# Kernel optimization log

Hardware: AMD Instinct MI355X
Metric: run time of the kernel (lower is better)

Reference implementation:

```python
import jax, jax.numpy as jnp
import numpy as np

N = 131072
IN_DIM = 12
HID = 256
NUM_LAYERS = 10
OUT_DIM = 3


def _xavier(key, fan_in, fan_out, gain):
    bound = gain * jnp.sqrt(6.0 / (fan_in + fan_out))
    return jax.random.uniform(key, (fan_in, fan_out), jnp.float32, -bound, bound)


def setup_inputs() -> dict:
    key = jax.random.key(0)
    ks = jax.random.split(key, 12)
    x = jax.random.normal(ks[0], (N, IN_DIM), jnp.float32)
    W0 = _xavier(ks[1], IN_DIM, HID, 5.0)
    b0 = jnp.zeros((HID,), jnp.float32)
    Ws = jnp.stack([_xavier(ks[2 + i], HID, HID, 5.0) for i in range(NUM_LAYERS - 1)])
    bs = jnp.zeros((NUM_LAYERS - 1, HID), jnp.float32)
    Wout = _xavier(ks[11], HID, OUT_DIM, 1.0)
    bout = jnp.zeros((OUT_DIM,), jnp.float32)
    return {"x": x, "W0": W0, "b0": b0, "Ws": Ws, "bs": bs, "Wout": Wout, "bout": bout}


def _act(h, i):
    m = i % 4
    if m == 0:
        return jnp.sin(h)
    if m == 1:
        return jnp.cos(h)
    if m == 2:
        return jnp.exp(-h * h)  # gaussian
    return jnp.tanh(h)


def reference(x, W0, b0, Ws, bs, Wout, bout):
    h = _act(x @ W0 + b0, 0)
    for i in range(1, NUM_LAYERS):  # small fixed layer loop
        h = _act(h @ Ws[i - 1] + bs[i - 1], i)
    return jax.nn.sigmoid(h @ Wout + bout)  # (N, 3) in [0, 1]
```

## Files before the change

kernel.cpp:

```cpp
#include <hip/hip_runtime.h>
#include <type_traits>

#define HID 256
#define PTS 64
typedef unsigned short ushort_t;
typedef unsigned int uint_t;
typedef __attribute__((ext_vector_type(8))) _Float16 half8v;
typedef __attribute__((ext_vector_type(4))) float f32x4;

#define LO_SCALE   4096.0f
#define LO_INV     0.000244140625f

__device__ __forceinline__ ushort_t h_bits(_Float16 h) { return __builtin_bit_cast(ushort_t, h); }

template <int M>
__device__ __forceinline__ float act(float z) {
    if constexpr (M == 0) return __sinf(z);
    else if constexpr (M == 1) return __cosf(z);
    else if constexpr (M == 2) return __expf(-z * z);
    else { float e = __expf(2.0f * z); return 1.0f - 2.0f / (e + 1.0f); }
}

#define NFRAG (9 * 8 * 16)
#define PREP_THREADS (NFRAG * 64)

__global__ void prep_w(const float* __restrict__ Ws,
                       _Float16* __restrict__ WHI, _Float16* __restrict__ WLO) {
    int t = blockIdx.x * 256 + threadIdx.x;
    if (t >= PREP_THREADS) return;
    int l  = t & 63;
    int f  = t >> 6;
    int ct = f & 15;
    int kt = (f >> 4) & 7;
    int L  = f >> 7;
    int col = ct * 16 + (l & 15);
    int kb  = kt * 32 + (l >> 4) * 8;
    const float* Wp = Ws + (size_t)L * 65536;
    _Float16* oh = WHI + (size_t)t * 8;
    _Float16* ol = WLO + (size_t)t * 8;
    #pragma unroll
    for (int j = 0; j < 8; ++j) {
        float wv = Wp[(size_t)(kb + j) * 256 + col];
        _Float16 hi = (_Float16)wv;
        oh[j] = hi;
        ol[j] = (_Float16)((wv - (float)hi) * LO_SCALE);
    }
}

__global__ __launch_bounds__(512, 4) void cppn_mfma(
    const float* __restrict__ x,
    const float* __restrict__ W0,
    const float* __restrict__ b0,
    const float* __restrict__ bs,
    const float* __restrict__ Wout,
    const float* __restrict__ bout,
    const _Float16* __restrict__ WHI,
    const _Float16* __restrict__ WLO,
    float* __restrict__ out,
    int n)
{
    __shared__ ushort_t ha[64 * 256];
    __shared__ ushort_t hb[64 * 256];

    const int tid = threadIdx.x;
    const int l   = tid & 63;
    const int w   = tid >> 6;
    const long p0 = (long)blockIdx.x * PTS;

    {
        const int p  = l;
        const long pg = p0 + p;
        float xv[12];
        if (pg < n) {
            const float4* xr = (const float4*)(x + pg * 12);
            float4 a = xr[0], b = xr[1], c = xr[2];
            xv[0]=a.x; xv[1]=a.y; xv[2]=a.z;  xv[3]=a.w;
            xv[4]=b.x; xv[5]=b.y; xv[6]=b.z;  xv[7]=b.w;
            xv[8]=c.x; xv[9]=c.y; xv[10]=c.z; xv[11]=c.w;
        } else {
            #pragma unroll
            for (int k = 0; k < 12; ++k) xv[k] = 0.0f;
        }
        const int jb = w * 32;
        float z[32];
        #pragma unroll
        for (int jj = 0; jj < 32; ++jj) z[jj] = b0[jb + jj];
        #pragma unroll
        for (int k = 0; k < 12; ++k) {
            const float a = xv[k];
            #pragma unroll
            for (int jj = 0; jj < 32; ++jj)
                z[jj] = fmaf(a, W0[k * HID + jb + jj], z[jj]);
        }
        const int swz = (p & 7) << 3;
        #pragma unroll
        for (int jj = 0; jj < 32; jj += 2) {
            float v0 = act<0>(z[jj]), v1 = act<0>(z[jj + 1]);
            _Float16 h0 = (_Float16)v0, h1 = (_Float16)v1;
            _Float16 l0 = (_Float16)((v0 - (float)h0) * LO_SCALE);
            _Float16 l1 = (_Float16)((v1 - (float)h1) * LO_SCALE);
            int ei = p * 256 + ((jb + jj) ^ swz);
            *(uint_t*)&ha[ei] = (uint_t)h_bits(h0) | ((uint_t)h_bits(h1) << 16);
            *(uint_t*)&hb[ei] = (uint_t)h_bits(l0) | ((uint_t)h_bits(l1) << 16);
        }
    }
    __syncthreads();

    const int lg   = l >> 4;
    const int lm   = l & 15;
    const int aswz = (l & 7) << 3;
    const int ab[4] = { (0*16+lm)*256, (1*16+lm)*256, (2*16+lm)*256, (3*16+lm)*256 };

    for (int Li = 0; Li < 9; ++Li) {
        const _Float16* __restrict__ WHL = WHI + (size_t)(Li * 8 * 16) * 512 + (size_t)l * 8;
        const _Float16* __restrict__ WLL = WLO + (size_t)(Li * 8 * 16) * 512 + (size_t)l * 8;

        f32x4 acc[4][2], accL[4][2];
        #pragma unroll
        for (int rt = 0; rt < 4; ++rt)
            #pragma unroll
            for (int c = 0; c < 2; ++c) {
                acc[rt][c]  = (f32x4){0.f, 0.f, 0.f, 0.f};
                accL[rt][c] = (f32x4){0.f, 0.f, 0.f, 0.f};
            }

        half8v bch[2], bcl[2];
        bch[0] = *(const half8v*)(WHL + (size_t)(w * 2 + 0) * 512);
        bch[1] = *(const half8v*)(WHL + (size_t)(w * 2 + 1) * 512);
        bcl[0] = *(const half8v*)(WLL + (size_t)(w * 2 + 0) * 512);
        bcl[1] = *(const half8v*)(WLL + (size_t)(w * 2 + 1) * 512);

        #pragma unroll 1
        for (int kt = 0; kt < 8; ++kt) {
            const int ktn = (kt + 1) & 7;
            half8v bnh[2], bnl[2];
            bnh[0] = *(const half8v*)(WHL + (size_t)(ktn * 16 + w * 2 + 0) * 512);
            bnh[1] = *(const half8v*)(WHL + (size_t)(ktn * 16 + w * 2 + 1) * 512);
            bnl[0] = *(const half8v*)(WLL + (size_t)(ktn * 16 + w * 2 + 0) * 512);
            bnl[1] = *(const half8v*)(WLL + (size_t)(ktn * 16 + w * 2 + 1) * 512);

            const int ke = (kt * 32 + lg * 8) ^ aswz;

            {
                half8v a_hi[2], a_lo[2];
                a_hi[0] = *(const half8v*)&ha[ab[0] + ke];
                a_hi[1] = *(const half8v*)&ha[ab[1] + ke];
                a_lo[0] = *(const half8v*)&hb[ab[0] + ke];
                a_lo[1] = *(const half8v*)&hb[ab[1] + ke];
                #pragma unroll
                for (int c = 0; c < 2; ++c)
                    #pragma unroll
                    for (int r = 0; r < 2; ++r)
                        acc[r][c] = __builtin_amdgcn_mfma_f32_16x16x32_f16(a_hi[r], bch[c], acc[r][c], 0, 0, 0);
                #pragma unroll
                for (int c = 0; c < 2; ++c)
                    #pragma unroll
                    for (int r = 0; r < 2; ++r)
                        accL[r][c] = __builtin_amdgcn_mfma_f32_16x16x32_f16(a_hi[r], bcl[c], accL[r][c], 0, 0, 0);
                #pragma unroll
                for (int c = 0; c < 2; ++c)
                    #pragma unroll
                    for (int r = 0; r < 2; ++r)
                        accL[r][c] = __builtin_amdgcn_mfma_f32_16x16x32_f16(a_lo[r], bch[c], accL[r][c], 0, 0, 0);
            }
            {
                half8v a_hi[2], a_lo[2];
                a_hi[0] = *(const half8v*)&ha[ab[2] + ke];
                a_hi[1] = *(const half8v*)&ha[ab[3] + ke];
                a_lo[0] = *(const half8v*)&hb[ab[2] + ke];
                a_lo[1] = *(const half8v*)&hb[ab[3] + ke];
                #pragma unroll
                for (int c = 0; c < 2; ++c)
                    #pragma unroll
                    for (int r = 0; r < 2; ++r)
                        acc[2+r][c] = __builtin_amdgcn_mfma_f32_16x16x32_f16(a_hi[r], bch[c], acc[2+r][c], 0, 0, 0);
                #pragma unroll
                for (int c = 0; c < 2; ++c)
                    #pragma unroll
                    for (int r = 0; r < 2; ++r)
                        accL[2+r][c] = __builtin_amdgcn_mfma_f32_16x16x32_f16(a_hi[r], bcl[c], accL[2+r][c], 0, 0, 0);
                #pragma unroll
                for (int c = 0; c < 2; ++c)
                    #pragma unroll
                    for (int r = 0; r < 2; ++r)
                        accL[2+r][c] = __builtin_amdgcn_mfma_f32_16x16x32_f16(a_lo[r], bch[c], accL[2+r][c], 0, 0, 0);
            }
            bch[0] = bnh[0]; bch[1] = bnh[1];
            bcl[0] = bnl[0]; bcl[1] = bnl[1];
        }
        __syncthreads();

        const float* bsL = bs + Li * 256;
        const int m = (Li + 1) & 3;
        auto storeact = [&](auto mt) {
            constexpr int M = decltype(mt)::value;
            #pragma unroll
            for (int c = 0; c < 2; ++c) {
                const int j  = w * 32 + c * 16 + lm;
                const float bj = bsL[j];
                #pragma unroll
                for (int rt = 0; rt < 4; ++rt) {
                    #pragma unroll
                    for (int r = 0; r < 4; ++r) {
                        const int p = rt * 16 + lg * 4 + r;
                        float zv = acc[rt][c][r] + accL[rt][c][r] * LO_INV + bj;
                        float v = act<M>(zv);
                        _Float16 vh = (_Float16)v;
                        _Float16 vl = (_Float16)((v - (float)vh) * LO_SCALE);
                        const int ei = p * 256 + (j ^ ((p & 7) << 3));
                        ha[ei] = h_bits(vh);
                        hb[ei] = h_bits(vl);
                    }
                }
            }
        };
        if      (m == 0) storeact(std::integral_constant<int,0>{});
        else if (m == 1) storeact(std::integral_constant<int,1>{});
        else if (m == 2) storeact(std::integral_constant<int,2>{});
        else             storeact(std::integral_constant<int,3>{});
        __syncthreads();
    }

    if (tid < 192) {
        const int p = tid & 63;
        const int c = tid >> 6;
        const long pg = p0 + p;
        if (pg < n) {
            const int swz = (p & 7) << 3;
            float zacc = bout[c];
            #pragma unroll 4
            for (int c2 = 0; c2 < 32; ++c2) {
                const int ei = p * 256 + ((c2 * 8) ^ swz);
                half8v vh = *(const half8v*)&ha[ei];
                half8v vl = *(const half8v*)&hb[ei];
                #pragma unroll
                for (int e = 0; e < 8; ++e) {
                    const int k = c2 * 8 + e;
                    float hv = (float)vh[e] + (float)vl[e] * LO_INV;
                    zacc = fmaf(hv, Wout[k * 3 + c], zacc);
                }
            }
            out[pg * 3 + c] = 1.0f / (1.0f + __expf(-zacc));
        }
    }
}

__global__ __launch_bounds__(512, 4) void cppn_fused_fp32(
    const float* __restrict__ x, const float* __restrict__ W0,
    const float* __restrict__ b0, const float* __restrict__ Ws,
    const float* __restrict__ bs, const float* __restrict__ Wout,
    const float* __restrict__ bout, float* __restrict__ out, int n)
{
    __shared__ float h[HID][PTS];
    const int tid  = threadIdx.x;
    const int p    = tid & 63;
    const int j0   = __builtin_amdgcn_readfirstlane((tid >> 6) << 5);
    const long pg  = (long)blockIdx.x * PTS + p;
    const bool live = (pg < n);
    {
        float xv[12];
        if (live) {
            const float4* xr = (const float4*)(x + pg * 12);
            float4 a = xr[0], b = xr[1], c = xr[2];
            xv[0]=a.x; xv[1]=a.y; xv[2]=a.z;  xv[3]=a.w;
            xv[4]=b.x; xv[5]=b.y; xv[6]=b.z;  xv[7]=b.w;
            xv[8]=c.x; xv[9]=c.y; xv[10]=c.z; xv[11]=c.w;
        } else {
            #pragma unroll
            for (int k = 0; k < 12; ++k) xv[k] = 0.0f;
        }
        float acc[32];
        #pragma unroll
        for (int q = 0; q < 32; ++q) acc[q] = 0.0f;
        #pragma unroll
        for (int k = 0; k < 12; ++k) {
            const float a = xv[k];
            const float4* wr = (const float4*)(W0 + k * HID + j0);
            #pragma unroll
            for (int q = 0; q < 8; ++q) {
                float4 wv = wr[q];
                acc[4*q+0] = fmaf(a, wv.x, acc[4*q+0]);
                acc[4*q+1] = fmaf(a, wv.y, acc[4*q+1]);
                acc[4*q+2] = fmaf(a, wv.z, acc[4*q+2]);
                acc[4*q+3] = fmaf(a, wv.w, acc[4*q+3]);
            }
        }
        #pragma unroll
        for (int q = 0; q < 8; ++q) {
            float4 b4 = *(const float4*)(b0 + j0 + 4*q);
            h[j0+4*q+0][p] = act<0>(acc[4*q+0] + b4.x);
            h[j0+4*q+1][p] = act<0>(acc[4*q+1] + b4.y);
            h[j0+4*q+2][p] = act<0>(acc[4*q+2] + b4.z);
            h[j0+4*q+3][p] = act<0>(acc[4*q+3] + b4.w);
        }
        __syncthreads();
    }
    auto layerF = [&](const float* __restrict__ W, const float* __restrict__ b, auto mtag) {
        constexpr int M = decltype(mtag)::value;
        float acc[32];
        #pragma unroll
        for (int q = 0; q < 32; ++q) acc[q] = 0.0f;
        #pragma unroll 2
        for (int k = 0; k < HID; ++k) {
            const float a = h[k][p];
            const float4* wr = (const float4*)(W + k * HID + j0);
            #pragma unroll
            for (int q = 0; q < 8; ++q) {
                float4 wv = wr[q];
                acc[4*q+0] = fmaf(a, wv.x, acc[4*q+0]);
                acc[4*q+1] = fmaf(a, wv.y, acc[4*q+1]);
                acc[4*q+2] = fmaf(a, wv.z, acc[4*q+2]);
                acc[4*q+3] = fmaf(a, wv.w, acc[4*q+3]);
            }
        }
        __syncthreads();
        #pragma unroll
        for (int q = 0; q < 8; ++q) {
            float4 b4 = *(const float4*)(b + j0 + 4*q);
            h[j0+4*q+0][p] = act<M>(acc[4*q+0] + b4.x);
            h[j0+4*q+1][p] = act<M>(acc[4*q+1] + b4.y);
            h[j0+4*q+2][p] = act<M>(acc[4*q+2] + b4.z);
            h[j0+4*q+3][p] = act<M>(acc[4*q+3] + b4.w);
        }
        __syncthreads();
    };
    layerF(Ws + 0*65536, bs + 0*256, std::integral_constant<int,1>{});
    layerF(Ws + 1*65536, bs + 1*256, std::integral_constant<int,2>{});
    layerF(Ws + 2*65536, bs + 2*256, std::integral_constant<int,3>{});
    layerF(Ws + 3*65536, bs + 3*256, std::integral_constant<int,0>{});
    layerF(Ws + 4*65536, bs + 4*256, std::integral_constant<int,1>{});
    layerF(Ws + 5*65536, bs + 5*256, std::integral_constant<int,2>{});
    layerF(Ws + 6*65536, bs + 6*256, std::integral_constant<int,3>{});
    layerF(Ws + 7*65536, bs + 7*256, std::integral_constant<int,0>{});
    layerF(Ws + 8*65536, bs + 8*256, std::integral_constant<int,1>{});
    if (tid < 192) {
        const int pp = tid & 63;
        const int c  = tid >> 6;
        const long pgo = (long)blockIdx.x * PTS + pp;
        if (pgo < n) {
            float z = bout[c];
            #pragma unroll 4
            for (int k = 0; k < HID; ++k)
                z = fmaf(h[k][pp], Wout[k * 3 + c], z);
            out[pgo * 3 + c] = 1.0f / (1.0f + __expf(-z));
        }
    }
}

extern "C" void kernel_launch(void* const* d_in, const int* in_sizes, int n_in,
                              void* d_out, int out_size, void* d_ws, size_t ws_size,
                              hipStream_t stream) {
    const float* x    = (const float*)d_in[0];
    const float* W0   = (const float*)d_in[1];
    const float* b0   = (const float*)d_in[2];
    const float* Ws   = (const float*)d_in[3];
    const float* bs   = (const float*)d_in[4];
    const float* Wout = (const float*)d_in[5];
    const float* bout = (const float*)d_in[6];
    float* out = (float*)d_out;

    const int n = in_sizes[0] / 12;
    const int grid = (n + PTS - 1) / PTS;

    const size_t whi_bytes = (size_t)PREP_THREADS * 8 * sizeof(_Float16);
    const size_t need = 2 * whi_bytes;

    if (ws_size >= need) {
        _Float16* WHI = (_Float16*)d_ws;
        _Float16* WLO = (_Float16*)((char*)d_ws + whi_bytes);
        prep_w<<<(PREP_THREADS + 255) / 256, 256, 0, stream>>>(Ws, WHI, WLO);
        cppn_mfma<<<grid, 512, 0, stream>>>(x, W0, b0, bs, Wout, bout, WHI, WLO, out, n);
    } else {
        cppn_fused_fp32<<<grid, 512, 0, stream>>>(x, W0, b0, Ws, bs, Wout, bout, out, n);
    }
}
```

Before: 469.9 us.

## Drop hi/lo split-fp16 MFMA in final layers and unroll layer loop

```diff
diff --git a/kernel.cpp b/kernel.cpp
--- a/kernel.cpp
+++ b/kernel.cpp
@@ -47,6 +47,142 @@
     }
 }
 
+template <int LI, int M, bool SPLITM, bool SPLITST>
+__device__ __forceinline__ void do_layer(
+    ushort_t* ha, ushort_t* hb,
+    const _Float16* __restrict__ WHI, const _Float16* __restrict__ WLO,
+    const float* __restrict__ bs,
+    int l, int w, int lg, int lm, int aswz)
+{
+    const _Float16* __restrict__ WHL = WHI + (size_t)(LI * 128) * 512 + (size_t)l * 8;
+    const _Float16* __restrict__ WLL = WLO + (size_t)(LI * 128) * 512 + (size_t)l * 8;
+    const float* bsL = bs + LI * 256;
+    const float bj0 = bsL[w * 32 + lm];
+    const float bj1 = bsL[w * 32 + 16 + lm];
+
+    const int ab0 = (0 * 16 + lm) * 256;
+    const int ab1 = (1 * 16 + lm) * 256;
+    const int ab2 = (2 * 16 + lm) * 256;
+    const int ab3 = (3 * 16 + lm) * 256;
+
+    f32x4 acc[4][2];
+    f32x4 accL[4][2];
+    #pragma unroll
+    for (int rt = 0; rt < 4; ++rt) {
+        acc[rt][0] = (f32x4){bj0, bj0, bj0, bj0};
+        acc[rt][1] = (f32x4){bj1, bj1, bj1, bj1};
+        if constexpr (SPLITM) {
+            accL[rt][0] = (f32x4){0.f, 0.f, 0.f, 0.f};
+            accL[rt][1] = (f32x4){0.f, 0.f, 0.f, 0.f};
+        }
+    }
+
+    half8v bch[2], bcl[2];
+    bch[0] = *(const half8v*)(WHL + (size_t)(w * 2 + 0) * 512);
+    bch[1] = *(const half8v*)(WHL + (size_t)(w * 2 + 1) * 512);
+    if constexpr (SPLITM) {
+        bcl[0] = *(const half8v*)(WLL + (size_t)(w * 2 + 0) * 512);
+        bcl[1] = *(const half8v*)(WLL + (size_t)(w * 2 + 1) * 512);
+    }
+
+    #pragma unroll 1
+    for (int kt = 0; kt < 8; ++kt) {
+        const int ktn = (kt + 1) & 7;
+        half8v bnh[2], bnl[2];
+        bnh[0] = *(const half8v*)(WHL + (size_t)(ktn * 16 + w * 2 + 0) * 512);
+        bnh[1] = *(const half8v*)(WHL + (size_t)(ktn * 16 + w * 2 + 1) * 512);
+        if constexpr (SPLITM) {
+            bnl[0] = *(const half8v*)(WLL + (size_t)(ktn * 16 + w * 2 + 0) * 512);
+            bnl[1] = *(const half8v*)(WLL + (size_t)(ktn * 16 + w * 2 + 1) * 512);
+        }
+        const int ke = (kt * 32 + lg * 8) ^ aswz;
+
+        if constexpr (SPLITM) {
+            {
+                half8v a_hi0 = *(const half8v*)&ha[ab0 + ke];
+                half8v a_hi1 = *(const half8v*)&ha[ab1 + ke];
+                half8v a_lo0 = *(const half8v*)&hb[ab0 + ke];
+                half8v a_lo1 = *(const half8v*)&hb[ab1 + ke];
+                #pragma unroll
+                for (int c = 0; c < 2; ++c) {
+                    acc[0][c]  = __builtin_amdgcn_mfma_f32_16x16x32_f16(a_hi0, bch[c], acc[0][c],  0, 0, 0);
+                    acc[1][c]  = __builtin_amdgcn_mfma_f32_16x16x32_f16(a_hi1, bch[c], acc[1][c],  0, 0, 0);
+                }
+                #pragma unroll
+                for (int c = 0; c < 2; ++c) {
+                    accL[0][c] = __builtin_amdgcn_mfma_f32_16x16x32_f16(a_hi0, bcl[c], accL[0][c], 0, 0, 0);
+                    accL[1][c] = __builtin_amdgcn_mfma_f32_16x16x32_f16(a_hi1, bcl[c], accL[1][c], 0, 0, 0);
+                }
+                #pragma unroll
+                for (int c = 0; c < 2; ++c) {
+                    accL[0][c] = __builtin_amdgcn_mfma_f32_16x16x32_f16(a_lo0, bch[c], accL[0][c], 0, 0, 0);
+                    accL[1][c] = __builtin_amdgcn_mfma_f32_16x16x32_f16(a_lo1, bch[c], accL[1][c], 0, 0, 0);
+                }
+            }
+            {
+                half8v a_hi0 = *(const half8v*)&ha[ab2 + ke];
+                half8v a_hi1 = *(const half8v*)&ha[ab3 + ke];
+                half8v a_lo0 = *(const half8v*)&hb[ab2 + ke];
+                half8v a_lo1 = *(const half8v*)&hb[ab3 + ke];
+                #pragma unroll
+                for (int c = 0; c < 2; ++c) {
+                    acc[2][c]  = __builtin_amdgcn_mfma_f32_16x16x32_f16(a_hi0, bch[c], acc[2][c],  0, 0, 0);
+                    acc[3][c]  = __builtin_amdgcn_mfma_f32_16x16x32_f16(a_hi1, bch[c], acc[3][c],  0, 0, 0);
+                }
+                #pragma unroll
+                for (int c = 0; c < 2; ++c) {
+                    accL[2][c] = __builtin_amdgcn_mfma_f32_16x16x32_f16(a_hi0, bcl[c], accL[2][c], 0, 0, 0);
+                    accL[3][c] = __builtin_amdgcn_mfma_f32_16x16x32_f16(a_hi1, bcl[c], accL[3][c], 0, 0, 0);
+                }
+                #pragma unroll
+                for (int c = 0; c < 2; ++c) {
+                    accL[2][c] = __builtin_amdgcn_mfma_f32_16x16x32_f16(a_lo0, bch[c], accL[2][c], 0, 0, 0);
+                    accL[3][c] = __builtin_amdgcn_mfma_f32_16x16x32_f16(a_lo1, bch[c], accL[3][c], 0, 0, 0);
+                }
+            }
+        } else {
+            half8v a0 = *(const half8v*)&ha[ab0 + ke];
+            half8v a1 = *(const half8v*)&ha[ab1 + ke];
+            half8v a2 = *(const half8v*)&ha[ab2 + ke];
+            half8v a3 = *(const half8v*)&ha[ab3 + ke];
+            #pragma unroll
+            for (int c = 0; c < 2; ++c) {
+                acc[0][c] = __builtin_amdgcn_mfma_f32_16x16x32_f16(a0, bch[c], acc[0][c], 0, 0, 0);
+                acc[1][c] = __builtin_amdgcn_mfma_f32_16x16x32_f16(a1, bch[c], acc[1][c], 0, 0, 0);
+                acc[2][c] = __builtin_amdgcn_mfma_f32_16x16x32_f16(a2, bch[c], acc[2][c], 0, 0, 0);
+                acc[3][c] = __builtin_amdgcn_mfma_f32_16x16x32_f16(a3, bch[c], acc[3][c], 0, 0, 0);
+            }
+        }
+
+        bch[0] = bnh[0]; bch[1] = bnh[1];
+        if constexpr (SPLITM) { bcl[0] = bnl[0]; bcl[1] = bnl[1]; }
+    }
+    __syncthreads();
+
+    #pragma unroll
+    for (int c = 0; c < 2; ++c) {
+        const int j = w * 32 + c * 16 + lm;
+        #pragma unroll
+        for (int rt = 0; rt < 4; ++rt) {
+            #pragma unroll
+            for (int r = 0; r < 4; ++r) {
+                const int p = rt * 16 + lg * 4 + r;
+                float zv;
+                if constexpr (SPLITM) zv = fmaf(accL[rt][c][r], LO_INV, acc[rt][c][r]);
+                else                  zv = acc[rt][c][r];
+                float v = act<M>(zv);
+                const int ei = p * 256 + (j ^ ((p & 7) << 3));
+                ha[ei] = h_bits((_Float16)v);
+                if constexpr (SPLITST) {
+                    _Float16 vh = (_Float16)v;
+                    hb[ei] = h_bits((_Float16)((v - (float)vh) * LO_SCALE));
+                }
+            }
+        }
+    }
+    __syncthreads();
+}
+
 __global__ __launch_bounds__(512, 4) void cppn_mfma(
     const float* __restrict__ x,
     const float* __restrict__ W0,
@@ -109,117 +245,16 @@
     const int lg   = l >> 4;
     const int lm   = l & 15;
     const int aswz = (l & 7) << 3;
-    const int ab[4] = { (0*16+lm)*256, (1*16+lm)*256, (2*16+lm)*256, (3*16+lm)*256 };
-
-    for (int Li = 0; Li < 9; ++Li) {
-        const _Float16* __restrict__ WHL = WHI + (size_t)(Li * 8 * 16) * 512 + (size_t)l * 8;
-        const _Float16* __restrict__ WLL = WLO + (size_t)(Li * 8 * 16) * 512 + (size_t)l * 8;
-
-        f32x4 acc[4][2], accL[4][2];
-        #pragma unroll
-        for (int rt = 0; rt < 4; ++rt)
-            #pragma unroll
-            for (int c = 0; c < 2; ++c) {
-                acc[rt][c]  = (f32x4){0.f, 0.f, 0.f, 0.f};
-                accL[rt][c] = (f32x4){0.f, 0.f, 0.f, 0.f};
-            }
-
-        half8v bch[2], bcl[2];
-        bch[0] = *(const half8v*)(WHL + (size_t)(w * 2 + 0) * 512);
-        bch[1] = *(const half8v*)(WHL + (size_t)(w * 2 + 1) * 512);
-        bcl[0] = *(const half8v*)(WLL + (size_t)(w * 2 + 0) * 512);
-        bcl[1] = *(const half8v*)(WLL + (size_t)(w * 2 + 1) * 512);
-
-        #pragma unroll 1
-        for (int kt = 0; kt < 8; ++kt) {
-            const int ktn = (kt + 1) & 7;
-            half8v bnh[2], bnl[2];
-            bnh[0] = *(const half8v*)(WHL + (size_t)(ktn * 16 + w * 2 + 0) * 512);
-            bnh[1] = *(const half8v*)(WHL + (size_t)(ktn * 16 + w * 2 + 1) * 512);
-            bnl[0] = *(const half8v*)(WLL + (size_t)(ktn * 16 + w * 2 + 0) * 512);
-            bnl[1] = *(const half8v*)(WLL + (size_t)(ktn * 16 + w * 2 + 1) * 512);
-
-            const int ke = (kt * 32 + lg * 8) ^ aswz;
-
-            {
-                half8v a_hi[2], a_lo[2];
-                a_hi[0] = *(const half8v*)&ha[ab[0] + ke];
-                a_hi[1] = *(const half8v*)&ha[ab[1] + ke];
-                a_lo[0] = *(const half8v*)&hb[ab[0] + ke];
-                a_lo[1] = *(const half8v*)&hb[ab[1] + ke];
-                #pragma unroll
-                for (int c = 0; c < 2; ++c)
-                    #pragma unroll
-                    for (int r = 0; r < 2; ++r)
-                        acc[r][c] = __builtin_amdgcn_mfma_f32_16x16x32_f16(a_hi[r], bch[c], acc[r][c], 0, 0, 0);
-                #pragma unroll
-                for (int c = 0; c < 2; ++c)
-                    #pragma unroll
-                    for (int r = 0; r < 2; ++r)
-                        accL[r][c] = __builtin_amdgcn_mfma_f32_16x16x32_f16(a_hi[r], bcl[c], accL[r][c], 0, 0, 0);
-                #pragma unroll
-                for (int c = 0; c < 2; ++c)
-                    #pragma unroll
-                    for (int r = 0; r < 2; ++r)
-                        accL[r][c] = __builtin_amdgcn_mfma_f32_16x16x32_f16(a_lo[r], bch[c], accL[r][c], 0, 0, 0);
-            }
-            {
-                half8v a_hi[2], a_lo[2];
-                a_hi[0] = *(const half8v*)&ha[ab[2] + ke];
-                a_hi[1] = *(const half8v*)&ha[ab[3] + ke];
-                a_lo[0] = *(const half8v*)&hb[ab[2] + ke];
-                a_lo[1] = *(const half8v*)&hb[ab[3] + ke];
-                #pragma unroll
-                for (int c = 0; c < 2; ++c)
-                    #pragma unroll
-                    for (int r = 0; r < 2; ++r)
-                        acc[2+r][c] = __builtin_amdgcn_mfma_f32_16x16x32_f16(a_hi[r], bch[c], acc[2+r][c], 0, 0, 0);
-                #pragma unroll
-                for (int c = 0; c < 2; ++c)
-                    #pragma unroll
-                    for (int r = 0; r < 2; ++r)
-                        accL[2+r][c] = __builtin_amdgcn_mfma_f32_16x16x32_f16(a_hi[r], bcl[c], accL[2+r][c], 0, 0, 0);
-                #pragma unroll
-                for (int c = 0; c < 2; ++c)
-                    #pragma unroll
-                    for (int r = 0; r < 2; ++r)
-                        accL[2+r][c] = __builtin_amdgcn_mfma_f32_16x16x32_f16(a_lo[r], bch[c], accL[2+r][c], 0, 0, 0);
-            }
-            bch[0] = bnh[0]; bch[1] = bnh[1];
-            bcl[0] = bnl[0]; bcl[1] = bnl[1];
-        }
-        __syncthreads();
-
-        const float* bsL = bs + Li * 256;
-        const int m = (Li + 1) & 3;
-        auto storeact = [&](auto mt) {
-            constexpr int M = decltype(mt)::value;
-            #pragma unroll
-            for (int c = 0; c < 2; ++c) {
-                const int j  = w * 32 + c * 16 + lm;
-                const float bj = bsL[j];
-                #pragma unroll
-                for (int rt = 0; rt < 4; ++rt) {
-                    #pragma unroll
-                    for (int r = 0; r < 4; ++r) {
-                        const int p = rt * 16 + lg * 4 + r;
-                        float zv = acc[rt][c][r] + accL[rt][c][r] * LO_INV + bj;
-                        float v = act<M>(zv);
-                        _Float16 vh = (_Float16)v;
-                        _Float16 vl = (_Float16)((v - (float)vh) * LO_SCALE);
-                        const int ei = p * 256 + (j ^ ((p & 7) << 3));
-                        ha[ei] = h_bits(vh);
-                        hb[ei] = h_bits(vl);
-                    }
-                }
-            }
-        };
-        if      (m == 0) storeact(std::integral_constant<int,0>{});
-        else if (m == 1) storeact(std::integral_constant<int,1>{});
-        else if (m == 2) storeact(std::integral_constant<int,2>{});
-        else             storeact(std::integral_constant<int,3>{});
-        __syncthreads();
-    }
+
+    do_layer<0, 1, true,  true >(ha, hb, WHI, WLO, bs, l, w, lg, lm, aswz);
+    do_layer<1, 2, true,  true >(ha, hb, WHI, WLO, bs, l, w, lg, lm, aswz);
+    do_layer<2, 3, true,  true >(ha, hb, WHI, WLO, bs, l, w, lg, lm, aswz);
+    do_layer<3, 0, true,  true >(ha, hb, WHI, WLO, bs, l, w, lg, lm, aswz);
+    do_layer<4, 1, true,  true >(ha, hb, WHI, WLO, bs, l, w, lg, lm, aswz);
+    do_layer<5, 2, true,  true >(ha, hb, WHI, WLO, bs, l, w, lg, lm, aswz);
+    do_layer<6, 3, true,  false>(ha, hb, WHI, WLO, bs, l, w, lg, lm, aswz);
+    do_layer<7, 0, false, false>(ha, hb, WHI, WLO, bs, l, w, lg, lm, aswz);
+    do_layer<8, 1, false, false>(ha, hb, WHI, WLO, bs, l, w, lg, lm, aswz);
 
     if (tid < 192) {
         const int p = tid & 63;
@@ -232,12 +267,10 @@
             for (int c2 = 0; c2 < 32; ++c2) {
                 const int ei = p * 256 + ((c2 * 8) ^ swz);
                 half8v vh = *(const half8v*)&ha[ei];
-                half8v vl = *(const half8v*)&hb[ei];
                 #pragma unroll
                 for (int e = 0; e < 8; ++e) {
                     const int k = c2 * 8 + e;
-                    float hv = (float)vh[e] + (float)vl[e] * LO_INV;
-                    zacc = fmaf(hv, Wout[k * 3 + c], zacc);
+                    zacc = fmaf((float)vh[e], Wout[k * 3 + c], zacc);
                 }
             }
             out[pg * 3 + c] = 1.0f / (1.0f + __expf(-zacc));
```

Measured after the change: 495.2 us. +5.4%, slower.
